# Performance work log

Measured on AMD Instinct MI355X. Metric: run time of the kernel, lower is better.

Reference implementation:

```python
import jax, jax.numpy as jnp
import numpy as np

EPS = 1e-5
SLOPE = 0.01  # torch LeakyReLU default negative_slope


def _stage(h, W):
    # h: [B, N, k, Cin]; W: [Cout, Cin] (1x1 conv, no bias)
    h = jnp.einsum('bnkc,oc->bnko', h, W)
    # InstanceNorm2d (affine=False): normalize per (batch, channel) over spatial (N, k)
    mean = jnp.mean(h, axis=(1, 2), keepdims=True)
    var = jnp.var(h, axis=(1, 2), keepdims=True)
    h = (h - mean) * jax.lax.rsqrt(var + EPS)
    return jnp.where(h >= 0, h, SLOPE * h)


def setup_inputs() -> dict:
    key = jax.random.key(0)
    k1, k2, k3, k4, k5 = jax.random.split(key, 5)
    B, N, D, K, C = 8, 4096, 64, 20, 64
    x = jax.random.normal(k1, (B, N, D), dtype=jnp.float32)
    ind = jax.random.randint(k2, (B, N, K), 0, B * N, dtype=jnp.int64)
    W1 = jax.random.normal(k3, (C, 2 * D), dtype=jnp.float32) * 0.05
    W2 = jax.random.normal(k4, (C, C), dtype=jnp.float32) * 0.05
    W3 = jax.random.normal(k5, (C, C), dtype=jnp.float32) * 0.05
    return {"x": x, "ind": ind, "W1": W1, "W2": W2, "W3": W3}


def reference(x, ind, W1, W2, W3):
    B, N, D = x.shape
    k = ind.shape[2]
    # Gather neighbors via global (B*N) indices, as in the torch code
    y = x.reshape(B * N, D)[ind.reshape(B * N, k)].reshape(B, N, k, D)  # [B,N,k,D]
    xe = jnp.broadcast_to(x[:, :, None, :], (B, N, k, D))
    feat = jnp.concatenate([y - xe, xe], axis=3)  # [B,N,k,2D]
    h = _stage(feat, W1)
    h = _stage(h, W2)
    h = _stage(h, W3)
    # max-pool over k neighbors -> [B, N, Cout]
    return jnp.max(h, axis=2)
```

## Files before the change

kernel.cpp:

```cpp
#include <hip/hip_runtime.h>

#define BDIM 8
#define NPTS 4096
#define KNEI 20
#define BN (BDIM*NPTS)
#define NKCNT (NPTS*KNEI)
#define EPSI 1e-5f
#define SLOPE 0.01f

typedef _Float16 half_t;
typedef __attribute__((ext_vector_type(2))) _Float16 h2v;
typedef __attribute__((ext_vector_type(4))) _Float16 h4v;
typedef __attribute__((ext_vector_type(8))) _Float16 h8v;
typedef __attribute__((ext_vector_type(4))) float f32x4;
typedef __attribute__((ext_vector_type(2))) float f32x2;

__device__ __forceinline__ h2v cvt2(float a, float b) {
    return __builtin_bit_cast(h2v, __builtin_amdgcn_cvt_pkrtz(a, b));
}
__device__ __forceinline__ unsigned long long pack4_f16(const f32x4& a) {
    unsigned p0 = __builtin_bit_cast(unsigned, cvt2(a[0], a[1]));
    unsigned p1 = __builtin_bit_cast(unsigned, cvt2(a[2], a[3]));
    return ((unsigned long long)p1 << 32) | p0;
}

__global__ __launch_bounds__(512) void k0_uv(const float* __restrict__ x,
        const float* __restrict__ W1, const float* __restrict__ W2,
        const float* __restrict__ W3, half_t* __restrict__ u,
        half_t* __restrict__ v, half_t* __restrict__ Wh2,
        half_t* __restrict__ Wh3) {
    int tid = threadIdx.x;
    if (blockIdx.x >= BN / 128) {
        const float* src = (tid < 256) ? W2 : W3;
        half_t* dst = (tid < 256) ? Wh2 : Wh3;
        int t = tid & 255;
        for (int i = t; i < 4096; i += 256) dst[i] = (half_t)src[i];
        return;
    }
    int lane = tid & 63, w = tid >> 6;
    int l15 = lane & 15, q = lane >> 4;
    int row = blockIdx.x * 128 + w * 16 + l15;
    h8v bx[2];
#pragma unroll
    for (int kc = 0; kc < 2; ++kc) {
        const float* xp = x + (size_t)row * 64 + kc * 32 + q * 8;
        f32x4 x0 = *(const f32x4*)xp;
        f32x4 x1 = *(const f32x4*)(xp + 4);
        h8v t;
#pragma unroll
        for (int j = 0; j < 4; ++j) { t[j] = (half_t)x0[j]; t[4 + j] = (half_t)x1[j]; }
        bx[kc] = t;
    }
    h8v wa[4][2], wd[4][2];
#pragma unroll
    for (int mt = 0; mt < 4; ++mt)
#pragma unroll
        for (int kc = 0; kc < 2; ++kc) {
            const float* wp = W1 + (mt * 16 + l15) * 128 + kc * 32 + q * 8;
            f32x4 a0 = *(const f32x4*)wp;
            f32x4 a1 = *(const f32x4*)(wp + 4);
            f32x4 b0 = *(const f32x4*)(wp + 64);
            f32x4 b1 = *(const f32x4*)(wp + 68);
            h8v ta, td;
#pragma unroll
            for (int j = 0; j < 4; ++j) {
                ta[j] = (half_t)a0[j]; ta[4 + j] = (half_t)a1[j];
                td[j] = (half_t)(b0[j] - a0[j]); td[4 + j] = (half_t)(b1[j] - a1[j]);
            }
            wa[mt][kc] = ta; wd[mt][kc] = td;
        }
#pragma unroll
    for (int mt = 0; mt < 4; ++mt) {
        f32x4 au = {0.f, 0.f, 0.f, 0.f}, av = {0.f, 0.f, 0.f, 0.f};
        au = __builtin_amdgcn_mfma_f32_16x16x32_f16(wa[mt][0], bx[0], au, 0, 0, 0);
        au = __builtin_amdgcn_mfma_f32_16x16x32_f16(wa[mt][1], bx[1], au, 0, 0, 0);
        av = __builtin_amdgcn_mfma_f32_16x16x32_f16(wd[mt][0], bx[0], av, 0, 0, 0);
        av = __builtin_amdgcn_mfma_f32_16x16x32_f16(wd[mt][1], bx[1], av, 0, 0, 0);
        *(unsigned long long*)(u + (size_t)row * 64 + mt * 16 + q * 4) = pack4_f16(au);
        *(unsigned long long*)(v + (size_t)row * 64 + mt * 16 + q * 4) = pack4_f16(av);
    }
}

__global__ __launch_bounds__(512) void k1_stats1(const half_t* __restrict__ u,
        const half_t* __restrict__ v, const int* __restrict__ ind,
        float* __restrict__ s1) {
    __shared__ float sacc[128];
    int tid = threadIdx.x;
    if (tid < 128) sacc[tid] = 0.f;
    int lane = tid & 63, w = tid >> 6;
    int b = blockIdx.x >> 7;
    int n0 = (blockIdx.x & 127) << 5;
    int p = b * NPTS + n0 + w * 4 + (lane >> 4);
    int rh = (lane >> 3) & 1, c8 = lane & 7;
    const int* ip = ind + (size_t)p * 20;
    int idx[10];
#pragma unroll
    for (int r = 0; r < 10; ++r) idx[r] = ip[r * 2 + rh];
    h8v vv = *(const h8v*)(v + (size_t)p * 64 + c8 * 8);
    h8v g[10];
#pragma unroll
    for (int r = 0; r < 10; ++r)
        g[r] = *(const h8v*)(u + (size_t)idx[r] * 64 + c8 * 8);
    float s[8] = {}, qa[8] = {};
#pragma unroll
    for (int r = 0; r < 10; ++r) {
        h8v h = g[r] + vv;
#pragma unroll
        for (int j = 0; j < 8; ++j) {
            float f = (float)h[j];
            s[j] += f; qa[j] = fmaf(f, f, qa[j]);
        }
    }
#pragma unroll
    for (int m = 8; m <= 32; m <<= 1)
#pragma unroll
        for (int j = 0; j < 8; ++j) {
            s[j] += __shfl_xor(s[j], m, 64);
            qa[j] += __shfl_xor(qa[j], m, 64);
        }
    __syncthreads();
    if ((lane & 56) == 0) {
#pragma unroll
        for (int j = 0; j < 8; ++j) {
            atomicAdd(&sacc[c8 * 8 + j], s[j]);
            atomicAdd(&sacc[64 + c8 * 8 + j], qa[j]);
        }
    }
    __syncthreads();
    if (tid < 128)
        atomicAdd(&s1[(tid >> 6) * 512 + b * 64 + (tid & 63)], sacc[tid]);
}

__global__ __launch_bounds__(512, 4) void k2_stats2(const half_t* __restrict__ u,
        const half_t* __restrict__ v, const int* __restrict__ ind,
        const half_t* __restrict__ Wh2, const float* __restrict__ s1,
        float* __restrict__ s2) {
    __shared__ float sacc[128];
    int tid = threadIdx.x;
    if (tid < 128) sacc[tid] = 0.f;
    int lane = tid & 63, w = tid >> 6;
    int l15 = lane & 15, q = lane >> 4;
    int b = blockIdx.x >> 7;
    int n0 = (blockIdx.x & 127) << 5;
    int base = b * NPTS + n0;
    int base20 = base * 20;
    int idxs[5];
#pragma unroll
    for (int nt = 0; nt < 5; ++nt)
        idxs[nt] = ind[base20 + w * 80 + l15 * 5 + nt];
    h8v ug[5][2];
#pragma unroll
    for (int nt = 0; nt < 5; ++nt) {
        const half_t* up = u + (size_t)idxs[nt] * 64 + q * 8;
        ug[nt][0] = *(const h8v*)up;
        ug[nt][1] = *(const h8v*)(up + 32);
    }
    int gp = base + w * 4 + (l15 >> 2);
    h8v vfr[2];
    vfr[0] = *(const h8v*)(v + (size_t)gp * 64 + q * 8);
    vfr[1] = *(const h8v*)(v + (size_t)gp * 64 + 32 + q * 8);
    h8v aw[4][2];
#pragma unroll
    for (int mt = 0; mt < 4; ++mt)
#pragma unroll
        for (int kc = 0; kc < 2; ++kc)
            aw[mt][kc] = *(const h8v*)(Wh2 + (mt * 16 + l15) * 64 + kc * 32 + q * 8);
    const float inv = 1.0f / (float)NKCNT;
    h8v r1v[2], vn[2];
#pragma unroll
    for (int kc = 0; kc < 2; ++kc) {
        const float* sp = s1 + b * 64 + kc * 32 + q * 8;
        f32x4 sm0 = *(const f32x4*)sp;
        f32x4 sm1 = *(const f32x4*)(sp + 4);
        f32x4 sq0 = *(const f32x4*)(sp + 512);
        f32x4 sq1 = *(const f32x4*)(sp + 516);
#pragma unroll
        for (int j = 0; j < 8; ++j) {
            float mm = (j < 4 ? sm0[j & 3] : sm1[j & 3]) * inv;
            float va = (j < 4 ? sq0[j & 3] : sq1[j & 3]) * inv - mm * mm;
            float rs = rsqrtf(va + EPSI);
            r1v[kc][j] = (half_t)rs;
            vn[kc][j] = (half_t)(((float)vfr[kc][j] - mm) * rs);
        }
    }
    float ss[4][4] = {}, sq[4][4] = {};
#pragma unroll
    for (int nt = 0; nt < 5; ++nt) {
        h8v t0 = ug[nt][0] * r1v[0] + vn[0];
        h8v t1 = ug[nt][1] * r1v[1] + vn[1];
        h8v b0 = __builtin_elementwise_max(t0, t0 * (half_t)SLOPE);
        h8v b1 = __builtin_elementwise_max(t1, t1 * (half_t)SLOPE);
#pragma unroll
        for (int mt = 0; mt < 4; ++mt) {
            f32x4 a = {0.f, 0.f, 0.f, 0.f};
            a = __builtin_amdgcn_mfma_f32_16x16x32_f16(aw[mt][0], b0, a, 0, 0, 0);
            a = __builtin_amdgcn_mfma_f32_16x16x32_f16(aw[mt][1], b1, a, 0, 0, 0);
#pragma unroll
            for (int j = 0; j < 4; ++j) {
                ss[mt][j] += a[j];
                sq[mt][j] = fmaf(a[j], a[j], sq[mt][j]);
            }
        }
    }
#pragma unroll
    for (int m = 1; m < 16; m <<= 1)
#pragma unroll
        for (int mt = 0; mt < 4; ++mt)
#pragma unroll
            for (int j = 0; j < 4; ++j) {
                ss[mt][j] += __shfl_xor(ss[mt][j], m, 64);
                sq[mt][j] += __shfl_xor(sq[mt][j], m, 64);
            }
    __syncthreads();
    if (l15 == 0) {
#pragma unroll
        for (int mt = 0; mt < 4; ++mt)
#pragma unroll
            for (int j = 0; j < 4; ++j) {
                atomicAdd(&sacc[mt * 16 + q * 4 + j], ss[mt][j]);
                atomicAdd(&sacc[64 + mt * 16 + q * 4 + j], sq[mt][j]);
            }
    }
    __syncthreads();
    if (tid < 128)
        atomicAdd(&s2[(tid >> 6) * 512 + b * 64 + (tid & 63)], sacc[tid]);
}

__global__ __launch_bounds__(512, 4) void k3_fused(const half_t* __restrict__ u,
        const half_t* __restrict__ v, const int* __restrict__ ind,
        const half_t* __restrict__ Wh2, const half_t* __restrict__ Wh3,
        const float* __restrict__ s1, const float* __restrict__ s2,
        float* __restrict__ s3, float* __restrict__ out) {
    __shared__ __align__(16) unsigned char wlds[16384];
    __shared__ __align__(16) unsigned char scr[32768];
    __shared__ float sacc[128];
    int tid = threadIdx.x;
    if (tid < 128) sacc[tid] = 0.f;
    int lane = tid & 63, w = tid >> 6;
    int l15 = lane & 15, q = lane >> 4;
    int rw7 = l15 & 7;
    int b = blockIdx.x >> 7;
    int n0 = (blockIdx.x & 127) << 5;
    int base = b * NPTS + n0;
    int base20 = base * 20;
    for (int i = tid; i < 512; i += 512) {
        int rw = i >> 3, ch = i & 7;
        *(h8v*)(wlds + rw * 128 + ((ch ^ (rw & 7)) << 4)) =
            *(const h8v*)(Wh2 + rw * 64 + ch * 8);
        *(h8v*)(wlds + 8192 + rw * 128 + ((ch ^ (rw & 7)) << 4)) =
            *(const h8v*)(Wh3 + rw * 64 + ch * 8);
    }
    int idxs[5];
#pragma unroll
    for (int nt = 0; nt < 5; ++nt)
        idxs[nt] = ind[base20 + w * 80 + l15 * 5 + nt];
    const half_t* up0 = u + (size_t)idxs[0] * 64 + q * 8;
    h8v cu0 = *(const h8v*)up0;
    h8v cu1 = *(const h8v*)(up0 + 32);
    int gp = base + w * 4 + (l15 >> 2);
    h8v vfr[2];
#pragma unroll
    for (int kc = 0; kc < 2; ++kc)
        vfr[kc] = *(const h8v*)(v + (size_t)gp * 64 + kc * 32 + q * 8);
    const float inv = 1.0f / (float)NKCNT;
    h8v r1v[2], vn[2], r2v[2], m2v[2];
#pragma unroll
    for (int kc = 0; kc < 2; ++kc) {
        const float* sp1 = s1 + b * 64 + kc * 32 + q * 8;
        const float* sp2 = s2 + b * 64 + kc * 32 + q * 8;
        f32x4 a0 = *(const f32x4*)sp1;
        f32x4 a1 = *(const f32x4*)(sp1 + 4);
        f32x4 b0 = *(const f32x4*)(sp1 + 512);
        f32x4 b1 = *(const f32x4*)(sp1 + 516);
        f32x4 c0 = *(const f32x4*)sp2;
        f32x4 c1 = *(const f32x4*)(sp2 + 4);
        f32x4 d0 = *(const f32x4*)(sp2 + 512);
        f32x4 d1 = *(const f32x4*)(sp2 + 516);
#pragma unroll
        for (int j = 0; j < 8; ++j) {
            float mm = (j < 4 ? a0[j & 3] : a1[j & 3]) * inv;
            float va = (j < 4 ? b0[j & 3] : b1[j & 3]) * inv - mm * mm;
            float rs = rsqrtf(va + EPSI);
            r1v[kc][j] = (half_t)rs;
            vn[kc][j] = (half_t)(((float)vfr[kc][j] - mm) * rs);
            float mm2 = (j < 4 ? c0[j & 3] : c1[j & 3]) * inv;
            float va2 = (j < 4 ? d0[j & 3] : d1[j & 3]) * inv - mm2 * mm2;
            float rs2 = rsqrtf(va2 + EPSI);
            r2v[kc][j] = (half_t)rs2;
            m2v[kc][j] = (half_t)(-mm2 * rs2);
        }
    }
    unsigned char* scrw0 = scr + w * 4096;
    __syncthreads();
    float ss[4][4] = {}, sq[4][4] = {};
    h2v pm[4][2];
#pragma unroll
    for (int mt = 0; mt < 4; ++mt)
#pragma unroll
        for (int r = 0; r < 2; ++r)
            pm[mt][r] = (h2v){(half_t)-65504.f, (half_t)-65504.f};
#pragma unroll
    for (int nt = 0; nt < 6; ++nt) {
        if (nt < 5) {
            h8v nx0, nx1;
            if (nt < 4) {
                const half_t* upn = u + (size_t)idxs[nt + 1] * 64 + q * 8;
                nx0 = *(const h8v*)upn;
                nx1 = *(const h8v*)(upn + 32);
            }
            unsigned char* scrw = scrw0 + (nt & 1) * 2048;
            h8v t0 = cu0 * r1v[0] + vn[0];
            h8v t1 = cu1 * r1v[1] + vn[1];
            h8v b0 = __builtin_elementwise_max(t0, t0 * (half_t)SLOPE);
            h8v b1 = __builtin_elementwise_max(t1, t1 * (half_t)SLOPE);
#pragma unroll
            for (int mt = 0; mt < 4; ++mt) {
                h8v w0 = *(const h8v*)(wlds + (mt * 16 + l15) * 128 + ((q ^ rw7) << 4));
                h8v w1 = *(const h8v*)(wlds + (mt * 16 + l15) * 128 + (((4 + q) ^ rw7) << 4));
                f32x4 a = {0.f, 0.f, 0.f, 0.f};
                a = __builtin_amdgcn_mfma_f32_16x16x32_f16(w0, b0, a, 0, 0, 0);
                a = __builtin_amdgcn_mfma_f32_16x16x32_f16(w1, b1, a, 0, 0, 0);
                *(unsigned long long*)(scrw + l15 * 128 +
                    (((mt * 2 + (q >> 1)) ^ rw7) << 4) + (q & 1) * 8) = pack4_f16(a);
            }
            if (nt < 4) { cu0 = nx0; cu1 = nx1; }
        }
        if (nt > 0) {
            int m = nt - 1;
            unsigned char* scrr = scrw0 + (m & 1) * 2048;
            h8v hr0 = *(const h8v*)(scrr + l15 * 128 + ((q ^ rw7) << 4));
            h8v hr1 = *(const h8v*)(scrr + l15 * 128 + (((4 + q) ^ rw7) << 4));
            h8v t0 = hr0 * r2v[0] + m2v[0];
            h8v t1 = hr1 * r2v[1] + m2v[1];
            h8v b0 = __builtin_elementwise_max(t0, t0 * (half_t)SLOPE);
            h8v b1 = __builtin_elementwise_max(t1, t1 * (half_t)SLOPE);
#pragma unroll
            for (int mt = 0; mt < 4; ++mt) {
                h8v w0 = *(const h8v*)(wlds + 8192 + (mt * 16 + l15) * 128 + ((q ^ rw7) << 4));
                h8v w1 = *(const h8v*)(wlds + 8192 + (mt * 16 + l15) * 128 + (((4 + q) ^ rw7) << 4));
                f32x4 a = {0.f, 0.f, 0.f, 0.f};
                a = __builtin_amdgcn_mfma_f32_16x16x32_f16(w0, b0, a, 0, 0, 0);
                a = __builtin_amdgcn_mfma_f32_16x16x32_f16(w1, b1, a, 0, 0, 0);
#pragma unroll
                for (int j = 0; j < 4; ++j) {
                    ss[mt][j] += a[j];
                    sq[mt][j] = fmaf(a[j], a[j], sq[mt][j]);
                }
                h2v p0 = cvt2(a[0], a[1]);
                h2v p1 = cvt2(a[2], a[3]);
                pm[mt][0] = __builtin_elementwise_max(pm[mt][0], p0);
                pm[mt][1] = __builtin_elementwise_max(pm[mt][1], p1);
            }
        }
    }
#pragma unroll
    for (int m = 1; m <= 2; m <<= 1)
#pragma unroll
        for (int mt = 0; mt < 4; ++mt)
#pragma unroll
            for (int r = 0; r < 2; ++r) {
                int t = __shfl_xor(__builtin_bit_cast(int, pm[mt][r]), m, 64);
                pm[mt][r] = __builtin_elementwise_max(pm[mt][r],
                               __builtin_bit_cast(h2v, t));
            }
    {
        int ms = l15 & 3;
        h2v sa = ms == 0 ? pm[0][0] : ms == 1 ? pm[1][0] : ms == 2 ? pm[2][0] : pm[3][0];
        h2v sb = ms == 0 ? pm[0][1] : ms == 1 ? pm[1][1] : ms == 2 ? pm[2][1] : pm[3][1];
        f32x4 o = {(float)sa[0], (float)sa[1], (float)sb[0], (float)sb[1]};
        *(f32x4*)(out + (size_t)gp * 64 + ms * 16 + q * 4) = o;
    }
#pragma unroll
    for (int m = 1; m < 16; m <<= 1)
#pragma unroll
        for (int mt = 0; mt < 4; ++mt)
#pragma unroll
            for (int j = 0; j < 4; ++j) {
                ss[mt][j] += __shfl_xor(ss[mt][j], m, 64);
                sq[mt][j] += __shfl_xor(sq[mt][j], m, 64);
            }
    if (l15 == 0) {
#pragma unroll
        for (int mt = 0; mt < 4; ++mt)
#pragma unroll
            for (int j = 0; j < 4; ++j) {
                atomicAdd(&sacc[mt * 16 + q * 4 + j], ss[mt][j]);
                atomicAdd(&sacc[64 + mt * 16 + q * 4 + j], sq[mt][j]);
            }
    }
    __syncthreads();
    if (tid < 128)
        atomicAdd(&s3[(tid >> 6) * 512 + b * 64 + (tid & 63)], sacc[tid]);
}

__global__ __launch_bounds__(256) void k4_final(float* __restrict__ out,
        const float* __restrict__ s3) {
    int idx = blockIdx.x * 256 + threadIdx.x;
    int c = idx & 63;
    int b = idx >> 18;
    const float inv = 1.0f / (float)NKCNT;
    float mm = s3[b * 64 + c] * inv;
    float vv = s3[512 + b * 64 + c] * inv - mm * mm;
    float r = rsqrtf(vv + EPSI);
    float val = (out[idx] - mm) * r;
    out[idx] = val >= 0.f ? val : SLOPE * val;
}

extern "C" void kernel_launch(void* const* d_in, const int* in_sizes, int n_in,
                              void* d_out, int out_size, void* d_ws, size_t ws_size,
                              hipStream_t stream) {
    const float* x   = (const float*)d_in[0];
    const int*   ind = (const int*)d_in[1];
    const float* W1  = (const float*)d_in[2];
    const float* W2  = (const float*)d_in[3];
    const float* W3  = (const float*)d_in[4];
    float* out = (float*)d_out;

    half_t* u   = (half_t*)d_ws;
    half_t* v   = u + (size_t)BN * 64;
    half_t* Wh2 = v + (size_t)BN * 64;
    half_t* Wh3 = Wh2 + 4096;
    float* stats = (float*)(Wh3 + 4096);
    float* s1 = stats;
    float* s2 = stats + 1024;
    float* s3 = stats + 2048;

    (void)hipMemsetAsync(stats, 0, 3 * 1024 * sizeof(float), stream);
    k0_uv<<<dim3(BN / 128 + 1), dim3(512), 0, stream>>>(x, W1, W2, W3, u, v, Wh2, Wh3);
    k1_stats1<<<dim3(BN / 32), dim3(512), 0, stream>>>(u, v, ind, s1);
    k2_stats2<<<dim3(BN / 32), dim3(512), 0, stream>>>(u, v, ind, Wh2, s1, s2);
    k3_fused<<<dim3(BN / 32), dim3(512), 0, stream>>>(u, v, ind, Wh2, Wh3, s1, s2, s3, out);
    k4_final<<<dim3(BN * 64 / 256), dim3(256), 0, stream>>>(out, s3);
}
```

Measured before the change: 172.4 us.

## Fuse all stages into one cooperative persistent kernel with grid syncs

Replaces the five separate kernel launches with a single cooperative kernel of 256 blocks that runs the u/v projection, the three statistics passes and the final normalization, separated by grid-wide syncs. Each block now loops over four sub-groups of 32 points, and the W2/W3 weights are loaded into LDS once per block rather than once per small block. This removes launch gaps and repeated per-block setup, at the cost of grid.sync overhead and far fewer resident waves (256 blocks of 512 threads), which lowers latency hiding for the random gathers.

```diff
diff --git a/kernel.cpp b/kernel.cpp
--- a/kernel.cpp
+++ b/kernel.cpp
@@ -1,4 +1,7 @@
 #include <hip/hip_runtime.h>
+#include <hip/hip_cooperative_groups.h>
+
+namespace cg = cooperative_groups;
 
 #define BDIM 8
 #define NPTS 4096
@@ -10,10 +13,8 @@
 
 typedef _Float16 half_t;
 typedef __attribute__((ext_vector_type(2))) _Float16 h2v;
-typedef __attribute__((ext_vector_type(4))) _Float16 h4v;
 typedef __attribute__((ext_vector_type(8))) _Float16 h8v;
 typedef __attribute__((ext_vector_type(4))) float f32x4;
-typedef __attribute__((ext_vector_type(2))) float f32x2;
 
 __device__ __forceinline__ h2v cvt2(float a, float b) {
     return __builtin_bit_cast(h2v, __builtin_amdgcn_cvt_pkrtz(a, b));
@@ -24,386 +25,391 @@
     return ((unsigned long long)p1 << 32) | p0;
 }
 
-__global__ __launch_bounds__(512) void k0_uv(const float* __restrict__ x,
-        const float* __restrict__ W1, const float* __restrict__ W2,
-        const float* __restrict__ W3, half_t* __restrict__ u,
-        half_t* __restrict__ v, half_t* __restrict__ Wh2,
-        half_t* __restrict__ Wh3) {
-    int tid = threadIdx.x;
-    if (blockIdx.x >= BN / 128) {
-        const float* src = (tid < 256) ? W2 : W3;
-        half_t* dst = (tid < 256) ? Wh2 : Wh3;
-        int t = tid & 255;
-        for (int i = t; i < 4096; i += 256) dst[i] = (half_t)src[i];
-        return;
-    }
-    int lane = tid & 63, w = tid >> 6;
-    int l15 = lane & 15, q = lane >> 4;
-    int row = blockIdx.x * 128 + w * 16 + l15;
-    h8v bx[2];
-#pragma unroll
-    for (int kc = 0; kc < 2; ++kc) {
-        const float* xp = x + (size_t)row * 64 + kc * 32 + q * 8;
-        f32x4 x0 = *(const f32x4*)xp;
-        f32x4 x1 = *(const f32x4*)(xp + 4);
-        h8v t;
-#pragma unroll
-        for (int j = 0; j < 4; ++j) { t[j] = (half_t)x0[j]; t[4 + j] = (half_t)x1[j]; }
-        bx[kc] = t;
-    }
-    h8v wa[4][2], wd[4][2];
-#pragma unroll
-    for (int mt = 0; mt < 4; ++mt)
-#pragma unroll
-        for (int kc = 0; kc < 2; ++kc) {
-            const float* wp = W1 + (mt * 16 + l15) * 128 + kc * 32 + q * 8;
-            f32x4 a0 = *(const f32x4*)wp;
-            f32x4 a1 = *(const f32x4*)(wp + 4);
-            f32x4 b0 = *(const f32x4*)(wp + 64);
-            f32x4 b1 = *(const f32x4*)(wp + 68);
-            h8v ta, td;
-#pragma unroll
-            for (int j = 0; j < 4; ++j) {
-                ta[j] = (half_t)a0[j]; ta[4 + j] = (half_t)a1[j];
-                td[j] = (half_t)(b0[j] - a0[j]); td[4 + j] = (half_t)(b1[j] - a1[j]);
-            }
-            wa[mt][kc] = ta; wd[mt][kc] = td;
-        }
-#pragma unroll
-    for (int mt = 0; mt < 4; ++mt) {
-        f32x4 au = {0.f, 0.f, 0.f, 0.f}, av = {0.f, 0.f, 0.f, 0.f};
-        au = __builtin_amdgcn_mfma_f32_16x16x32_f16(wa[mt][0], bx[0], au, 0, 0, 0);
-        au = __builtin_amdgcn_mfma_f32_16x16x32_f16(wa[mt][1], bx[1], au, 0, 0, 0);
-        av = __builtin_amdgcn_mfma_f32_16x16x32_f16(wd[mt][0], bx[0], av, 0, 0, 0);
-        av = __builtin_amdgcn_mfma_f32_16x16x32_f16(wd[mt][1], bx[1], av, 0, 0, 0);
-        *(unsigned long long*)(u + (size_t)row * 64 + mt * 16 + q * 4) = pack4_f16(au);
-        *(unsigned long long*)(v + (size_t)row * 64 + mt * 16 + q * 4) = pack4_f16(av);
-    }
-}
-
-__global__ __launch_bounds__(512) void k1_stats1(const half_t* __restrict__ u,
-        const half_t* __restrict__ v, const int* __restrict__ ind,
-        float* __restrict__ s1) {
-    __shared__ float sacc[128];
-    int tid = threadIdx.x;
-    if (tid < 128) sacc[tid] = 0.f;
-    int lane = tid & 63, w = tid >> 6;
-    int b = blockIdx.x >> 7;
-    int n0 = (blockIdx.x & 127) << 5;
-    int p = b * NPTS + n0 + w * 4 + (lane >> 4);
-    int rh = (lane >> 3) & 1, c8 = lane & 7;
-    const int* ip = ind + (size_t)p * 20;
-    int idx[10];
-#pragma unroll
-    for (int r = 0; r < 10; ++r) idx[r] = ip[r * 2 + rh];
-    h8v vv = *(const h8v*)(v + (size_t)p * 64 + c8 * 8);
-    h8v g[10];
-#pragma unroll
-    for (int r = 0; r < 10; ++r)
-        g[r] = *(const h8v*)(u + (size_t)idx[r] * 64 + c8 * 8);
-    float s[8] = {}, qa[8] = {};
-#pragma unroll
-    for (int r = 0; r < 10; ++r) {
-        h8v h = g[r] + vv;
-#pragma unroll
-        for (int j = 0; j < 8; ++j) {
-            float f = (float)h[j];
-            s[j] += f; qa[j] = fmaf(f, f, qa[j]);
-        }
-    }
-#pragma unroll
-    for (int m = 8; m <= 32; m <<= 1)
-#pragma unroll
-        for (int j = 0; j < 8; ++j) {
-            s[j] += __shfl_xor(s[j], m, 64);
-            qa[j] += __shfl_xor(qa[j], m, 64);
-        }
-    __syncthreads();
-    if ((lane & 56) == 0) {
-#pragma unroll
-        for (int j = 0; j < 8; ++j) {
-            atomicAdd(&sacc[c8 * 8 + j], s[j]);
-            atomicAdd(&sacc[64 + c8 * 8 + j], qa[j]);
-        }
-    }
-    __syncthreads();
-    if (tid < 128)
-        atomicAdd(&s1[(tid >> 6) * 512 + b * 64 + (tid & 63)], sacc[tid]);
-}
-
-__global__ __launch_bounds__(512, 4) void k2_stats2(const half_t* __restrict__ u,
-        const half_t* __restrict__ v, const int* __restrict__ ind,
-        const half_t* __restrict__ Wh2, const float* __restrict__ s1,
-        float* __restrict__ s2) {
-    __shared__ float sacc[128];
-    int tid = threadIdx.x;
-    if (tid < 128) sacc[tid] = 0.f;
-    int lane = tid & 63, w = tid >> 6;
-    int l15 = lane & 15, q = lane >> 4;
-    int b = blockIdx.x >> 7;
-    int n0 = (blockIdx.x & 127) << 5;
-    int base = b * NPTS + n0;
-    int base20 = base * 20;
-    int idxs[5];
-#pragma unroll
-    for (int nt = 0; nt < 5; ++nt)
-        idxs[nt] = ind[base20 + w * 80 + l15 * 5 + nt];
-    h8v ug[5][2];
-#pragma unroll
-    for (int nt = 0; nt < 5; ++nt) {
-        const half_t* up = u + (size_t)idxs[nt] * 64 + q * 8;
-        ug[nt][0] = *(const h8v*)up;
-        ug[nt][1] = *(const h8v*)(up + 32);
-    }
-    int gp = base + w * 4 + (l15 >> 2);
-    h8v vfr[2];
-    vfr[0] = *(const h8v*)(v + (size_t)gp * 64 + q * 8);
-    vfr[1] = *(const h8v*)(v + (size_t)gp * 64 + 32 + q * 8);
-    h8v aw[4][2];
-#pragma unroll
-    for (int mt = 0; mt < 4; ++mt)
-#pragma unroll
-        for (int kc = 0; kc < 2; ++kc)
-            aw[mt][kc] = *(const h8v*)(Wh2 + (mt * 16 + l15) * 64 + kc * 32 + q * 8);
-    const float inv = 1.0f / (float)NKCNT;
-    h8v r1v[2], vn[2];
-#pragma unroll
-    for (int kc = 0; kc < 2; ++kc) {
-        const float* sp = s1 + b * 64 + kc * 32 + q * 8;
-        f32x4 sm0 = *(const f32x4*)sp;
-        f32x4 sm1 = *(const f32x4*)(sp + 4);
-        f32x4 sq0 = *(const f32x4*)(sp + 512);
-        f32x4 sq1 = *(const f32x4*)(sp + 516);
-#pragma unroll
-        for (int j = 0; j < 8; ++j) {
-            float mm = (j < 4 ? sm0[j & 3] : sm1[j & 3]) * inv;
-            float va = (j < 4 ? sq0[j & 3] : sq1[j & 3]) * inv - mm * mm;
-            float rs = rsqrtf(va + EPSI);
-            r1v[kc][j] = (half_t)rs;
-            vn[kc][j] = (half_t)(((float)vfr[kc][j] - mm) * rs);
-        }
-    }
-    float ss[4][4] = {}, sq[4][4] = {};
-#pragma unroll
-    for (int nt = 0; nt < 5; ++nt) {
-        h8v t0 = ug[nt][0] * r1v[0] + vn[0];
-        h8v t1 = ug[nt][1] * r1v[1] + vn[1];
-        h8v b0 = __builtin_elementwise_max(t0, t0 * (half_t)SLOPE);
-        h8v b1 = __builtin_elementwise_max(t1, t1 * (half_t)SLOPE);
-#pragma unroll
-        for (int mt = 0; mt < 4; ++mt) {
-            f32x4 a = {0.f, 0.f, 0.f, 0.f};
-            a = __builtin_amdgcn_mfma_f32_16x16x32_f16(aw[mt][0], b0, a, 0, 0, 0);
-            a = __builtin_amdgcn_mfma_f32_16x16x32_f16(aw[mt][1], b1, a, 0, 0, 0);
-#pragma unroll
-            for (int j = 0; j < 4; ++j) {
-                ss[mt][j] += a[j];
-                sq[mt][j] = fmaf(a[j], a[j], sq[mt][j]);
-            }
-        }
-    }
-#pragma unroll
-    for (int m = 1; m < 16; m <<= 1)
-#pragma unroll
-        for (int mt = 0; mt < 4; ++mt)
-#pragma unroll
-            for (int j = 0; j < 4; ++j) {
-                ss[mt][j] += __shfl_xor(ss[mt][j], m, 64);
-                sq[mt][j] += __shfl_xor(sq[mt][j], m, 64);
-            }
-    __syncthreads();
-    if (l15 == 0) {
-#pragma unroll
-        for (int mt = 0; mt < 4; ++mt)
-#pragma unroll
-            for (int j = 0; j < 4; ++j) {
-                atomicAdd(&sacc[mt * 16 + q * 4 + j], ss[mt][j]);
-                atomicAdd(&sacc[64 + mt * 16 + q * 4 + j], sq[mt][j]);
-            }
-    }
-    __syncthreads();
-    if (tid < 128)
-        atomicAdd(&s2[(tid >> 6) * 512 + b * 64 + (tid & 63)], sacc[tid]);
-}
-
-__global__ __launch_bounds__(512, 4) void k3_fused(const half_t* __restrict__ u,
-        const half_t* __restrict__ v, const int* __restrict__ ind,
-        const half_t* __restrict__ Wh2, const half_t* __restrict__ Wh3,
-        const float* __restrict__ s1, const float* __restrict__ s2,
+__global__ __launch_bounds__(512, 2) void mega(const float* __restrict__ x,
+        const int* __restrict__ ind, const float* __restrict__ W1,
+        const float* __restrict__ W2, const float* __restrict__ W3,
+        half_t* __restrict__ u, half_t* __restrict__ v,
+        half_t* __restrict__ Wh2, half_t* __restrict__ Wh3,
+        float* __restrict__ s1, float* __restrict__ s2,
         float* __restrict__ s3, float* __restrict__ out) {
+    cg::grid_group grid = cg::this_grid();
     __shared__ __align__(16) unsigned char wlds[16384];
     __shared__ __align__(16) unsigned char scr[32768];
     __shared__ float sacc[128];
     int tid = threadIdx.x;
-    if (tid < 128) sacc[tid] = 0.f;
     int lane = tid & 63, w = tid >> 6;
     int l15 = lane & 15, q = lane >> 4;
     int rw7 = l15 & 7;
-    int b = blockIdx.x >> 7;
-    int n0 = (blockIdx.x & 127) << 5;
-    int base = b * NPTS + n0;
-    int base20 = base * 20;
-    for (int i = tid; i < 512; i += 512) {
-        int rw = i >> 3, ch = i & 7;
-        *(h8v*)(wlds + rw * 128 + ((ch ^ (rw & 7)) << 4)) =
-            *(const h8v*)(Wh2 + rw * 64 + ch * 8);
-        *(h8v*)(wlds + 8192 + rw * 128 + ((ch ^ (rw & 7)) << 4)) =
-            *(const h8v*)(Wh3 + rw * 64 + ch * 8);
+    int bid = blockIdx.x;
+    int b = bid >> 5;
+    const float inv = 1.0f / (float)NKCNT;
+
+    {
+        int row = bid * 128 + w * 16 + l15;
+        h8v bx[2];
+#pragma unroll
+        for (int kc = 0; kc < 2; ++kc) {
+            const float* xp = x + (size_t)row * 64 + kc * 32 + q * 8;
+            f32x4 x0 = *(const f32x4*)xp;
+            f32x4 x1 = *(const f32x4*)(xp + 4);
+            h8v t;
+#pragma unroll
+            for (int j = 0; j < 4; ++j) { t[j] = (half_t)x0[j]; t[4 + j] = (half_t)x1[j]; }
+            bx[kc] = t;
+        }
+        h8v wa[4][2], wd[4][2];
+#pragma unroll
+        for (int mt = 0; mt < 4; ++mt)
+#pragma unroll
+            for (int kc = 0; kc < 2; ++kc) {
+                const float* wp = W1 + (mt * 16 + l15) * 128 + kc * 32 + q * 8;
+                f32x4 a0 = *(const f32x4*)wp;
+                f32x4 a1 = *(const f32x4*)(wp + 4);
+                f32x4 b0 = *(const f32x4*)(wp + 64);
+                f32x4 b1 = *(const f32x4*)(wp + 68);
+                h8v ta, td;
+#pragma unroll
+                for (int j = 0; j < 4; ++j) {
+                    ta[j] = (half_t)a0[j]; ta[4 + j] = (half_t)a1[j];
+                    td[j] = (half_t)(b0[j] - a0[j]); td[4 + j] = (half_t)(b1[j] - a1[j]);
+                }
+                wa[mt][kc] = ta; wd[mt][kc] = td;
+            }
+#pragma unroll
+        for (int mt = 0; mt < 4; ++mt) {
+            f32x4 au = {0.f, 0.f, 0.f, 0.f}, av = {0.f, 0.f, 0.f, 0.f};
+            au = __builtin_amdgcn_mfma_f32_16x16x32_f16(wa[mt][0], bx[0], au, 0, 0, 0);
+            au = __builtin_amdgcn_mfma_f32_16x16x32_f16(wa[mt][1], bx[1], au, 0, 0, 0);
+            av = __builtin_amdgcn_mfma_f32_16x16x32_f16(wd[mt][0], bx[0], av, 0, 0, 0);
+            av = __builtin_amdgcn_mfma_f32_16x16x32_f16(wd[mt][1], bx[1], av, 0, 0, 0);
+            *(unsigned long long*)(u + (size_t)row * 64 + mt * 16 + q * 4) = pack4_f16(au);
+            *(unsigned long long*)(v + (size_t)row * 64 + mt * 16 + q * 4) = pack4_f16(av);
+        }
+        if (bid == 0) {
+            for (int i = tid; i < 4096; i += 512) {
+                Wh2[i] = (half_t)W2[i];
+                Wh3[i] = (half_t)W3[i];
+            }
+        }
     }
-    int idxs[5];
-#pragma unroll
-    for (int nt = 0; nt < 5; ++nt)
-        idxs[nt] = ind[base20 + w * 80 + l15 * 5 + nt];
-    const half_t* up0 = u + (size_t)idxs[0] * 64 + q * 8;
-    h8v cu0 = *(const h8v*)up0;
-    h8v cu1 = *(const h8v*)(up0 + 32);
-    int gp = base + w * 4 + (l15 >> 2);
-    h8v vfr[2];
-#pragma unroll
-    for (int kc = 0; kc < 2; ++kc)
-        vfr[kc] = *(const h8v*)(v + (size_t)gp * 64 + kc * 32 + q * 8);
-    const float inv = 1.0f / (float)NKCNT;
-    h8v r1v[2], vn[2], r2v[2], m2v[2];
-#pragma unroll
-    for (int kc = 0; kc < 2; ++kc) {
-        const float* sp1 = s1 + b * 64 + kc * 32 + q * 8;
-        const float* sp2 = s2 + b * 64 + kc * 32 + q * 8;
-        f32x4 a0 = *(const f32x4*)sp1;
-        f32x4 a1 = *(const f32x4*)(sp1 + 4);
-        f32x4 b0 = *(const f32x4*)(sp1 + 512);
-        f32x4 b1 = *(const f32x4*)(sp1 + 516);
-        f32x4 c0 = *(const f32x4*)sp2;
-        f32x4 c1 = *(const f32x4*)(sp2 + 4);
-        f32x4 d0 = *(const f32x4*)(sp2 + 512);
-        f32x4 d1 = *(const f32x4*)(sp2 + 516);
-#pragma unroll
-        for (int j = 0; j < 8; ++j) {
-            float mm = (j < 4 ? a0[j & 3] : a1[j & 3]) * inv;
-            float va = (j < 4 ? b0[j & 3] : b1[j & 3]) * inv - mm * mm;
-            float rs = rsqrtf(va + EPSI);
-            r1v[kc][j] = (half_t)rs;
-            vn[kc][j] = (half_t)(((float)vfr[kc][j] - mm) * rs);
-            float mm2 = (j < 4 ? c0[j & 3] : c1[j & 3]) * inv;
-            float va2 = (j < 4 ? d0[j & 3] : d1[j & 3]) * inv - mm2 * mm2;
-            float rs2 = rsqrtf(va2 + EPSI);
-            r2v[kc][j] = (half_t)rs2;
-            m2v[kc][j] = (half_t)(-mm2 * rs2);
-        }
+    __threadfence();
+    grid.sync();
+    __threadfence();
+
+    {
+        if (tid < 128) sacc[tid] = 0.f;
+        int rh = (lane >> 3) & 1, c8 = lane & 7;
+        float s[8] = {}, qa[8] = {};
+#pragma unroll
+        for (int sg = 0; sg < 4; ++sg) {
+            int p = bid * 128 + sg * 32 + w * 4 + (lane >> 4);
+            const int* ip = ind + (size_t)p * 20;
+            int idx[10];
+#pragma unroll
+            for (int r = 0; r < 10; ++r) idx[r] = ip[r * 2 + rh];
+            h8v vv = *(const h8v*)(v + (size_t)p * 64 + c8 * 8);
+            h8v g[10];
+#pragma unroll
+            for (int r = 0; r < 10; ++r)
+                g[r] = *(const h8v*)(u + (size_t)idx[r] * 64 + c8 * 8);
+#pragma unroll
+            for (int r = 0; r < 10; ++r) {
+                h8v h = g[r] + vv;
+#pragma unroll
+                for (int j = 0; j < 8; ++j) {
+                    float f = (float)h[j];
+                    s[j] += f; qa[j] = fmaf(f, f, qa[j]);
+                }
+            }
+        }
+#pragma unroll
+        for (int m = 8; m <= 32; m <<= 1)
+#pragma unroll
+            for (int j = 0; j < 8; ++j) {
+                s[j] += __shfl_xor(s[j], m, 64);
+                qa[j] += __shfl_xor(qa[j], m, 64);
+            }
+        __syncthreads();
+        if ((lane & 56) == 0) {
+#pragma unroll
+            for (int j = 0; j < 8; ++j) {
+                atomicAdd(&sacc[c8 * 8 + j], s[j]);
+                atomicAdd(&sacc[64 + c8 * 8 + j], qa[j]);
+            }
+        }
+        __syncthreads();
+        if (tid < 128)
+            atomicAdd(&s1[(tid >> 6) * 512 + b * 64 + (tid & 63)], sacc[tid]);
     }
-    unsigned char* scrw0 = scr + w * 4096;
-    __syncthreads();
-    float ss[4][4] = {}, sq[4][4] = {};
-    h2v pm[4][2];
-#pragma unroll
-    for (int mt = 0; mt < 4; ++mt)
-#pragma unroll
-        for (int r = 0; r < 2; ++r)
-            pm[mt][r] = (h2v){(half_t)-65504.f, (half_t)-65504.f};
-#pragma unroll
-    for (int nt = 0; nt < 6; ++nt) {
-        if (nt < 5) {
-            h8v nx0, nx1;
-            if (nt < 4) {
-                const half_t* upn = u + (size_t)idxs[nt + 1] * 64 + q * 8;
-                nx0 = *(const h8v*)upn;
-                nx1 = *(const h8v*)(upn + 32);
-            }
-            unsigned char* scrw = scrw0 + (nt & 1) * 2048;
-            h8v t0 = cu0 * r1v[0] + vn[0];
-            h8v t1 = cu1 * r1v[1] + vn[1];
-            h8v b0 = __builtin_elementwise_max(t0, t0 * (half_t)SLOPE);
-            h8v b1 = __builtin_elementwise_max(t1, t1 * (half_t)SLOPE);
-#pragma unroll
-            for (int mt = 0; mt < 4; ++mt) {
-                h8v w0 = *(const h8v*)(wlds + (mt * 16 + l15) * 128 + ((q ^ rw7) << 4));
-                h8v w1 = *(const h8v*)(wlds + (mt * 16 + l15) * 128 + (((4 + q) ^ rw7) << 4));
-                f32x4 a = {0.f, 0.f, 0.f, 0.f};
-                a = __builtin_amdgcn_mfma_f32_16x16x32_f16(w0, b0, a, 0, 0, 0);
-                a = __builtin_amdgcn_mfma_f32_16x16x32_f16(w1, b1, a, 0, 0, 0);
-                *(unsigned long long*)(scrw + l15 * 128 +
-                    (((mt * 2 + (q >> 1)) ^ rw7) << 4) + (q & 1) * 8) = pack4_f16(a);
-            }
-            if (nt < 4) { cu0 = nx0; cu1 = nx1; }
-        }
-        if (nt > 0) {
-            int m = nt - 1;
-            unsigned char* scrr = scrw0 + (m & 1) * 2048;
-            h8v hr0 = *(const h8v*)(scrr + l15 * 128 + ((q ^ rw7) << 4));
-            h8v hr1 = *(const h8v*)(scrr + l15 * 128 + (((4 + q) ^ rw7) << 4));
-            h8v t0 = hr0 * r2v[0] + m2v[0];
-            h8v t1 = hr1 * r2v[1] + m2v[1];
-            h8v b0 = __builtin_elementwise_max(t0, t0 * (half_t)SLOPE);
-            h8v b1 = __builtin_elementwise_max(t1, t1 * (half_t)SLOPE);
-#pragma unroll
-            for (int mt = 0; mt < 4; ++mt) {
-                h8v w0 = *(const h8v*)(wlds + 8192 + (mt * 16 + l15) * 128 + ((q ^ rw7) << 4));
-                h8v w1 = *(const h8v*)(wlds + 8192 + (mt * 16 + l15) * 128 + (((4 + q) ^ rw7) << 4));
-                f32x4 a = {0.f, 0.f, 0.f, 0.f};
-                a = __builtin_amdgcn_mfma_f32_16x16x32_f16(w0, b0, a, 0, 0, 0);
-                a = __builtin_amdgcn_mfma_f32_16x16x32_f16(w1, b1, a, 0, 0, 0);
+    __threadfence();
+    grid.sync();
+    __threadfence();
+
+    {
+        if (tid < 128) sacc[tid] = 0.f;
+        h8v aw[4][2];
+#pragma unroll
+        for (int mt = 0; mt < 4; ++mt)
+#pragma unroll
+            for (int kc = 0; kc < 2; ++kc)
+                aw[mt][kc] = *(const h8v*)(Wh2 + (mt * 16 + l15) * 64 + kc * 32 + q * 8);
+        h8v r1v[2], m1b[2];
+#pragma unroll
+        for (int kc = 0; kc < 2; ++kc) {
+            const float* sp = s1 + b * 64 + kc * 32 + q * 8;
+            f32x4 sm0 = *(const f32x4*)sp;
+            f32x4 sm1 = *(const f32x4*)(sp + 4);
+            f32x4 sq0 = *(const f32x4*)(sp + 512);
+            f32x4 sq1 = *(const f32x4*)(sp + 516);
+#pragma unroll
+            for (int j = 0; j < 8; ++j) {
+                float mm = (j < 4 ? sm0[j & 3] : sm1[j & 3]) * inv;
+                float va = (j < 4 ? sq0[j & 3] : sq1[j & 3]) * inv - mm * mm;
+                float rs = rsqrtf(va + EPSI);
+                r1v[kc][j] = (half_t)rs;
+                m1b[kc][j] = (half_t)(-mm * rs);
+            }
+        }
+        float ss[4][4] = {}, sq[4][4] = {};
+#pragma unroll
+        for (int sg = 0; sg < 4; ++sg) {
+            int base = bid * 128 + sg * 32;
+            int base20 = base * 20;
+            int idxs[5];
+#pragma unroll
+            for (int nt = 0; nt < 5; ++nt)
+                idxs[nt] = ind[base20 + w * 80 + l15 * 5 + nt];
+            h8v ug[5][2];
+#pragma unroll
+            for (int nt = 0; nt < 5; ++nt) {
+                const half_t* up = u + (size_t)idxs[nt] * 64 + q * 8;
+                ug[nt][0] = *(const h8v*)up;
+                ug[nt][1] = *(const h8v*)(up + 32);
+            }
+            int gp = base + w * 4 + (l15 >> 2);
+            h8v vfr0 = *(const h8v*)(v + (size_t)gp * 64 + q * 8);
+            h8v vfr1 = *(const h8v*)(v + (size_t)gp * 64 + 32 + q * 8);
+            h8v vn[2];
+            vn[0] = vfr0 * r1v[0] + m1b[0];
+            vn[1] = vfr1 * r1v[1] + m1b[1];
+#pragma unroll
+            for (int nt = 0; nt < 5; ++nt) {
+                h8v t0 = ug[nt][0] * r1v[0] + vn[0];
+                h8v t1 = ug[nt][1] * r1v[1] + vn[1];
+                h8v b0 = __builtin_elementwise_max(t0, t0 * (half_t)SLOPE);
+                h8v b1 = __builtin_elementwise_max(t1, t1 * (half_t)SLOPE);
+#pragma unroll
+                for (int mt = 0; mt < 4; ++mt) {
+                    f32x4 a = {0.f, 0.f, 0.f, 0.f};
+                    a = __builtin_amdgcn_mfma_f32_16x16x32_f16(aw[mt][0], b0, a, 0, 0, 0);
+                    a = __builtin_amdgcn_mfma_f32_16x16x32_f16(aw[mt][1], b1, a, 0, 0, 0);
+#pragma unroll
+                    for (int j = 0; j < 4; ++j) {
+                        ss[mt][j] += a[j];
+                        sq[mt][j] = fmaf(a[j], a[j], sq[mt][j]);
+                    }
+                }
+            }
+        }
+#pragma unroll
+        for (int m = 1; m < 16; m <<= 1)
+#pragma unroll
+            for (int mt = 0; mt < 4; ++mt)
 #pragma unroll
                 for (int j = 0; j < 4; ++j) {
-                    ss[mt][j] += a[j];
-                    sq[mt][j] = fmaf(a[j], a[j], sq[mt][j]);
-                }
-                h2v p0 = cvt2(a[0], a[1]);
-                h2v p1 = cvt2(a[2], a[3]);
-                pm[mt][0] = __builtin_elementwise_max(pm[mt][0], p0);
-                pm[mt][1] = __builtin_elementwise_max(pm[mt][1], p1);
-            }
-        }
+                    ss[mt][j] += __shfl_xor(ss[mt][j], m, 64);
+                    sq[mt][j] += __shfl_xor(sq[mt][j], m, 64);
+                }
+        __syncthreads();
+        if (l15 == 0) {
+#pragma unroll
+            for (int mt = 0; mt < 4; ++mt)
+#pragma unroll
+                for (int j = 0; j < 4; ++j) {
+                    atomicAdd(&sacc[mt * 16 + q * 4 + j], ss[mt][j]);
+                    atomicAdd(&sacc[64 + mt * 16 + q * 4 + j], sq[mt][j]);
+                }
+        }
+        __syncthreads();
+        if (tid < 128)
+            atomicAdd(&s2[(tid >> 6) * 512 + b * 64 + (tid & 63)], sacc[tid]);
     }
-#pragma unroll
-    for (int m = 1; m <= 2; m <<= 1)
-#pragma unroll
-        for (int mt = 0; mt < 4; ++mt)
-#pragma unroll
-            for (int r = 0; r < 2; ++r) {
-                int t = __shfl_xor(__builtin_bit_cast(int, pm[mt][r]), m, 64);
-                pm[mt][r] = __builtin_elementwise_max(pm[mt][r],
-                               __builtin_bit_cast(h2v, t));
-            }
+    __threadfence();
+    grid.sync();
+    __threadfence();
+
     {
-        int ms = l15 & 3;
-        h2v sa = ms == 0 ? pm[0][0] : ms == 1 ? pm[1][0] : ms == 2 ? pm[2][0] : pm[3][0];
-        h2v sb = ms == 0 ? pm[0][1] : ms == 1 ? pm[1][1] : ms == 2 ? pm[2][1] : pm[3][1];
-        f32x4 o = {(float)sa[0], (float)sa[1], (float)sb[0], (float)sb[1]};
-        *(f32x4*)(out + (size_t)gp * 64 + ms * 16 + q * 4) = o;
+        if (tid < 128) sacc[tid] = 0.f;
+        {
+            int rw = tid >> 3, ch = tid & 7;
+            *(h8v*)(wlds + rw * 128 + ((ch ^ (rw & 7)) << 4)) =
+                *(const h8v*)(Wh2 + rw * 64 + ch * 8);
+            *(h8v*)(wlds + 8192 + rw * 128 + ((ch ^ (rw & 7)) << 4)) =
+                *(const h8v*)(Wh3 + rw * 64 + ch * 8);
+        }
+        h8v r1v[2], m1b[2], r2v[2], m2v[2];
+#pragma unroll
+        for (int kc = 0; kc < 2; ++kc) {
+            const float* sp1 = s1 + b * 64 + kc * 32 + q * 8;
+            const float* sp2 = s2 + b * 64 + kc * 32 + q * 8;
+            f32x4 a0 = *(const f32x4*)sp1;
+            f32x4 a1 = *(const f32x4*)(sp1 + 4);
+            f32x4 b0 = *(const f32x4*)(sp1 + 512);
+            f32x4 b1 = *(const f32x4*)(sp1 + 516);
+            f32x4 c0 = *(const f32x4*)sp2;
+            f32x4 c1 = *(const f32x4*)(sp2 + 4);
+            f32x4 d0 = *(const f32x4*)(sp2 + 512);
+            f32x4 d1 = *(const f32x4*)(sp2 + 516);
+#pragma unroll
+            for (int j = 0; j < 8; ++j) {
+                float mm = (j < 4 ? a0[j & 3] : a1[j & 3]) * inv;
+                float va = (j < 4 ? b0[j & 3] : b1[j & 3]) * inv - mm * mm;
+                float rs = rsqrtf(va + EPSI);
+                r1v[kc][j] = (half_t)rs;
+                m1b[kc][j] = (half_t)(-mm * rs);
+                float mm2 = (j < 4 ? c0[j & 3] : c1[j & 3]) * inv;
+                float va2 = (j < 4 ? d0[j & 3] : d1[j & 3]) * inv - mm2 * mm2;
+                float rs2 = rsqrtf(va2 + EPSI);
+                r2v[kc][j] = (half_t)rs2;
+                m2v[kc][j] = (half_t)(-mm2 * rs2);
+            }
+        }
+        unsigned char* scrw0 = scr + w * 4096;
+        int t3 = w >> 2, w4 = w & 3;
+        __syncthreads();
+        float ss[4][4] = {}, sq[4][4] = {};
+#pragma unroll
+        for (int sg = 0; sg < 4; ++sg) {
+            int base_t = bid * 128 + sg * 32 + t3 * 16;
+            int base20 = base_t * 20;
+            int idxs[5];
+#pragma unroll
+            for (int nt = 0; nt < 5; ++nt)
+                idxs[nt] = ind[base20 + w4 * 80 + l15 * 5 + nt];
+            const half_t* up0 = u + (size_t)idxs[0] * 64 + q * 8;
+            h8v cu0 = *(const h8v*)up0;
+            h8v cu1 = *(const h8v*)(up0 + 32);
+            int gp = base_t + w4 * 4 + (l15 >> 2);
+            h8v vfr0 = *(const h8v*)(v + (size_t)gp * 64 + q * 8);
+            h8v vfr1 = *(const h8v*)(v + (size_t)gp * 64 + 32 + q * 8);
+            h8v vn[2];
+            vn[0] = vfr0 * r1v[0] + m1b[0];
+            vn[1] = vfr1 * r1v[1] + m1b[1];
+            h2v pm[4][2];
+#pragma unroll
+            for (int mt = 0; mt < 4; ++mt)
+#pragma unroll
+                for (int r = 0; r < 2; ++r)
+                    pm[mt][r] = (h2v){(half_t)-65504.f, (half_t)-65504.f};
+#pragma unroll
+            for (int nt = 0; nt < 6; ++nt) {
+                if (nt < 5) {
+                    h8v nx0, nx1;
+                    if (nt < 4) {
+                        const half_t* upn = u + (size_t)idxs[nt + 1] * 64 + q * 8;
+                        nx0 = *(const h8v*)upn;
+                        nx1 = *(const h8v*)(upn + 32);
+                    }
+                    unsigned char* scrw = scrw0 + (nt & 1) * 2048;
+                    h8v t0 = cu0 * r1v[0] + vn[0];
+                    h8v t1 = cu1 * r1v[1] + vn[1];
+                    h8v b0 = __builtin_elementwise_max(t0, t0 * (half_t)SLOPE);
+                    h8v b1 = __builtin_elementwise_max(t1, t1 * (half_t)SLOPE);
+#pragma unroll
+                    for (int mt = 0; mt < 4; ++mt) {
+                        h8v w0 = *(const h8v*)(wlds + (mt * 16 + l15) * 128 + ((q ^ rw7) << 4));
+                        h8v w1 = *(const h8v*)(wlds + (mt * 16 + l15) * 128 + (((4 + q) ^ rw7) << 4));
+                        f32x4 a = {0.f, 0.f, 0.f, 0.f};
+                        a = __builtin_amdgcn_mfma_f32_16x16x32_f16(w0, b0, a, 0, 0, 0);
+                        a = __builtin_amdgcn_mfma_f32_16x16x32_f16(w1, b1, a, 0, 0, 0);
+                        *(unsigned long long*)(scrw + l15 * 128 +
+                            (((mt * 2 + (q >> 1)) ^ rw7) << 4) + (q & 1) * 8) = pack4_f16(a);
+                    }
+                    if (nt < 4) { cu0 = nx0; cu1 = nx1; }
+                }
+                if (nt > 0) {
+                    int m = nt - 1;
+                    unsigned char* scrr = scrw0 + (m & 1) * 2048;
+                    h8v hr0 = *(const h8v*)(scrr + l15 * 128 + ((q ^ rw7) << 4));
+                    h8v hr1 = *(const h8v*)(scrr + l15 * 128 + (((4 + q) ^ rw7) << 4));
+                    h8v t0 = hr0 * r2v[0] + m2v[0];
+                    h8v t1 = hr1 * r2v[1] + m2v[1];
+                    h8v b0 = __builtin_elementwise_max(t0, t0 * (half_t)SLOPE);
+                    h8v b1 = __builtin_elementwise_max(t1, t1 * (half_t)SLOPE);
+#pragma unroll
+                    for (int mt = 0; mt < 4; ++mt) {
+                        h8v w0 = *(const h8v*)(wlds + 8192 + (mt * 16 + l15) * 128 + ((q ^ rw7) << 4));
+                        h8v w1 = *(const h8v*)(wlds + 8192 + (mt * 16 + l15) * 128 + (((4 + q) ^ rw7) << 4));
+                        f32x4 a = {0.f, 0.f, 0.f, 0.f};
+                        a = __builtin_amdgcn_mfma_f32_16x16x32_f16(w0, b0, a, 0, 0, 0);
+                        a = __builtin_amdgcn_mfma_f32_16x16x32_f16(w1, b1, a, 0, 0, 0);
+#pragma unroll
+                        for (int j = 0; j < 4; ++j) {
+                            ss[mt][j] += a[j];
+                            sq[mt][j] = fmaf(a[j], a[j], sq[mt][j]);
+                        }
+                        h2v p0 = cvt2(a[0], a[1]);
+                        h2v p1 = cvt2(a[2], a[3]);
+                        pm[mt][0] = __builtin_elementwise_max(pm[mt][0], p0);
+                        pm[mt][1] = __builtin_elementwise_max(pm[mt][1], p1);
+                    }
+                }
+            }
+#pragma unroll
+            for (int m = 1; m <= 2; m <<= 1)
+#pragma unroll
+                for (int mt = 0; mt < 4; ++mt)
+#pragma unroll
+                    for (int r = 0; r < 2; ++r) {
+                        int t = __shfl_xor(__builtin_bit_cast(int, pm[mt][r]), m, 64);
+                        pm[mt][r] = __builtin_elementwise_max(pm[mt][r],
+                                       __builtin_bit_cast(h2v, t));
+                    }
+            int ms = l15 & 3;
+            h2v sa = ms == 0 ? pm[0][0] : ms == 1 ? pm[1][0] : ms == 2 ? pm[2][0] : pm[3][0];
+            h2v sb = ms == 0 ? pm[0][1] : ms == 1 ? pm[1][1] : ms == 2 ? pm[2][1] : pm[3][1];
+            f32x4 o = {(float)sa[0], (float)sa[1], (float)sb[0], (float)sb[1]};
+            *(f32x4*)(out + (size_t)gp * 64 + ms * 16 + q * 4) = o;
+        }
+#pragma unroll
+        for (int m = 1; m < 16; m <<= 1)
+#pragma unroll
+            for (int mt = 0; mt < 4; ++mt)
+#pragma unroll
+                for (int j = 0; j < 4; ++j) {
+                    ss[mt][j] += __shfl_xor(ss[mt][j], m, 64);
+                    sq[mt][j] += __shfl_xor(sq[mt][j], m, 64);
+                }
+        if (l15 == 0) {
+#pragma unroll
+            for (int mt = 0; mt < 4; ++mt)
+#pragma unroll
+                for (int j = 0; j < 4; ++j) {
+                    atomicAdd(&sacc[mt * 16 + q * 4 + j], ss[mt][j]);
+                    atomicAdd(&sacc[64 + mt * 16 + q * 4 + j], sq[mt][j]);
+                }
+        }
+        __syncthreads();
+        if (tid < 128)
+            atomicAdd(&s3[(tid >> 6) * 512 + b * 64 + (tid & 63)], sacc[tid]);
     }
-#pragma unroll
-    for (int m = 1; m < 16; m <<= 1)
-#pragma unroll
-        for (int mt = 0; mt < 4; ++mt)
-#pragma unroll
-            for (int j = 0; j < 4; ++j) {
-                ss[mt][j] += __shfl_xor(ss[mt][j], m, 64);
-                sq[mt][j] += __shfl_xor(sq[mt][j], m, 64);
-            }
-    if (l15 == 0) {
-#pragma unroll
-        for (int mt = 0; mt < 4; ++mt)
-#pragma unroll
-            for (int j = 0; j < 4; ++j) {
-                atomicAdd(&sacc[mt * 16 + q * 4 + j], ss[mt][j]);
-                atomicAdd(&sacc[64 + mt * 16 + q * 4 + j], sq[mt][j]);
-            }
+    __threadfence();
+    grid.sync();
+    __threadfence();
+
+    {
+#pragma unroll
+        for (int i = 0; i < 16; ++i) {
+            int idx = bid * 8192 + i * 512 + tid;
+            int c = idx & 63;
+            int b4 = idx >> 18;
+            float mm = s3[b4 * 64 + c] * inv;
+            float vv = s3[512 + b4 * 64 + c] * inv - mm * mm;
+            float r = rsqrtf(vv + EPSI);
+            float val = (out[idx] - mm) * r;
+            out[idx] = val >= 0.f ? val : SLOPE * val;
+        }
     }
-    __syncthreads();
-    if (tid < 128)
-        atomicAdd(&s3[(tid >> 6) * 512 + b * 64 + (tid & 63)], sacc[tid]);
-}
-
-__global__ __launch_bounds__(256) void k4_final(float* __restrict__ out,
-        const float* __restrict__ s3) {
-    int idx = blockIdx.x * 256 + threadIdx.x;
-    int c = idx & 63;
-    int b = idx >> 18;
-    const float inv = 1.0f / (float)NKCNT;
-    float mm = s3[b * 64 + c] * inv;
-    float vv = s3[512 + b * 64 + c] * inv - mm * mm;
-    float r = rsqrtf(vv + EPSI);
-    float val = (out[idx] - mm) * r;
-    out[idx] = val >= 0.f ? val : SLOPE * val;
 }
 
 extern "C" void kernel_launch(void* const* d_in, const int* in_sizes, int n_in,
@@ -426,9 +432,7 @@
     float* s3 = stats + 2048;
 
     (void)hipMemsetAsync(stats, 0, 3 * 1024 * sizeof(float), stream);
-    k0_uv<<<dim3(BN / 128 + 1), dim3(512), 0, stream>>>(x, W1, W2, W3, u, v, Wh2, Wh3);
-    k1_stats1<<<dim3(BN / 32), dim3(512), 0, stream>>>(u, v, ind, s1);
-    k2_stats2<<<dim3(BN / 32), dim3(512), 0, stream>>>(u, v, ind, Wh2, s1, s2);
-    k3_fused<<<dim3(BN / 32), dim3(512), 0, stream>>>(u, v, ind, Wh2, Wh3, s1, s2, s3, out);
-    k4_final<<<dim3(BN * 64 / 256), dim3(256), 0, stream>>>(out, s3);
+    void* args[] = {&x, &ind, &W1, &W2, &W3, &u, &v, &Wh2, &Wh3, &s1, &s2, &s3, &out};
+    (void)hipLaunchCooperativeKernel((const void*)mega, dim3(256), dim3(512),
+                                     args, 0, stream);
 }
```

Result: slower. 562.4 us (+226.3%).
